# Kernel tuning notes

Hardware: AMD Instinct MI355X
Metric: run time of the kernel (lower is better)

Reference implementation:

```python
import jax, jax.numpy as jnp
import numpy as np

HIDDEN = 1024
NUM_HEADS = 16
HEAD_DIM = HIDDEN // NUM_HEADS
ROPE_BASE = 10000.0
LN_EPS = 1e-8


def _rope_cos_sin(seq_len, dim, dtype=jnp.float32):
    inv_freq = 1.0 / (ROPE_BASE ** (jnp.arange(0, dim, 2, dtype=jnp.float32) / dim))
    t = jnp.arange(seq_len, dtype=jnp.float32)
    freqs = jnp.einsum('i,j->ij', t, inv_freq)          # [S, dim/2]
    emb = jnp.concatenate([freqs, freqs], axis=-1)       # [S, dim]
    return jnp.cos(emb).astype(dtype), jnp.sin(emb).astype(dtype)


def _rotate_half(x):
    x1, x2 = jnp.split(x, 2, axis=-1)
    return jnp.concatenate([-x2, x1], axis=-1)


def setup_inputs() -> dict:
    key = jax.random.key(0)
    ks = jax.random.split(key, 8)
    B, S, H = 4, 2048, HIDDEN
    x = jax.random.normal(ks[0], (B, S, H), dtype=jnp.float32)
    # causal mask, True = attend
    attn_mask = jnp.tril(jnp.ones((S, S), dtype=bool))[None].repeat(B, axis=0)
    lim_p = 1.0 / np.sqrt(H)
    Wp = jax.random.uniform(ks[1], (H, 4 * H), minval=-lim_p, maxval=lim_p, dtype=jnp.float32)
    bp = jax.random.uniform(ks[2], (4 * H,), minval=-lim_p, maxval=lim_p, dtype=jnp.float32)
    ln_g = jnp.ones((H,), dtype=jnp.float32)
    ln_b = jnp.zeros((H,), dtype=jnp.float32)
    Wt = jax.random.uniform(ks[3], (H, H), minval=-lim_p, maxval=lim_p, dtype=jnp.float32)
    bt = jax.random.uniform(ks[4], (H,), minval=-lim_p, maxval=lim_p, dtype=jnp.float32)
    return {"x": x, "attn_mask": attn_mask, "Wp": Wp, "bp": bp,
            "ln_g": ln_g, "ln_b": ln_b, "Wt": Wt, "bt": bt}


def reference(x, attn_mask, Wp, bp, ln_g, ln_b, Wt, bt):
    B, S, H = x.shape
    nh, hd = NUM_HEADS, HEAD_DIM
    proj = x @ Wp + bp                                   # [B,S,4H]
    U, V, Q, K = jnp.split(proj, 4, axis=-1)
    # [B, nh, S, hd]
    Q = Q.reshape(B, S, nh, hd).transpose(0, 2, 1, 3)
    K = K.reshape(B, S, nh, hd).transpose(0, 2, 1, 3)
    V = V.reshape(B, S, nh, hd).transpose(0, 2, 1, 3)
    cos, sin = _rope_cos_sin(S, hd, x.dtype)             # [S, hd]
    Qr = Q * cos + _rotate_half(Q) * sin
    Kr = K * cos + _rotate_half(K) * sin
    scale = hd ** -0.5
    scores = jnp.einsum('bhqd,bhkd->bhqk', Qr, Kr) * scale
    # masked positions -> sigmoid(-inf) == 0; use where for grad safety
    attn = jnp.where(attn_mask[:, None, :, :], jax.nn.sigmoid(scores), 0.0)
    attn_out = jnp.einsum('bhqk,bhkd->bhqd', attn, V)
    attn_out = attn_out.transpose(0, 2, 1, 3).reshape(B, S, H)
    mu = jnp.mean(attn_out, axis=-1, keepdims=True)
    var = jnp.var(attn_out, axis=-1, keepdims=True)
    attn_out = (attn_out - mu) / jnp.sqrt(var + LN_EPS) * ln_g + ln_b
    gated = jax.nn.silu(U) * attn_out
    out = gated @ Wt + bt
    return x + out
```

## Files before the change

### kernel.cpp

```cpp
#include <hip/hip_runtime.h>
#include <math.h>

#define H 1024
#define NH 16
#define HD 64
#define B_ 4
#define S_ 2048
#define ROWS (B_*S_)

#define QSCALE (-0.1803368801111664f)

typedef __bf16 bf16x2_t __attribute__((ext_vector_type(2)));
typedef __bf16 bf16x4_t __attribute__((ext_vector_type(4)));
typedef __bf16 bf16x8_t __attribute__((ext_vector_type(8)));
typedef float floatx4_t __attribute__((ext_vector_type(4)));

#define GLOAD_LDS16(gp, lp)                                                        \
    __builtin_amdgcn_global_load_lds(                                              \
        (const __attribute__((address_space(1))) unsigned int*)(gp),               \
        (__attribute__((address_space(3))) unsigned int*)(lp), 16, 0, 0)

__global__ __launch_bounds__(256)
void convert_x(const float* __restrict__ src, __bf16* __restrict__ dst)
{
    int i = blockIdx.x * blockDim.x + threadIdx.x;
    float4 v = *reinterpret_cast<const float4*>(&src[(size_t)i * 4]);
    bf16x4_t w = { (__bf16)v.x, (__bf16)v.y, (__bf16)v.z, (__bf16)v.w };
    *reinterpret_cast<bf16x4_t*>(&dst[(size_t)i * 4]) = w;
}

__global__ __launch_bounds__(256)
void transpose_cvt(const float* __restrict__ W, __bf16* __restrict__ Wt, int K, int N)
{
    __shared__ __bf16 t[32][33];
    const int tx = threadIdx.x & 31, ty = threadIdx.x >> 5;
    const int bn = blockIdx.x * 32, bk = blockIdx.y * 32;
#pragma unroll
    for (int i = 0; i < 4; i++) {
        int r = ty + i * 8;
        t[tx][r] = (__bf16)W[(size_t)(bk + r) * N + bn + tx];
    }
    __syncthreads();
#pragma unroll
    for (int i = 0; i < 4; i++) {
        int r = ty + i * 8;
        Wt[(size_t)(bn + r) * K + bk + tx] = t[r][tx];
    }
}

template<typename OUT_T, bool RESID>
__global__ __launch_bounds__(256)
void gemm_mfma(const __bf16* __restrict__ A, const __bf16* __restrict__ Bt,
               const float* __restrict__ bias, const float* __restrict__ resid,
               OUT_T* __restrict__ C, int M, int N, int K)
{
    __shared__ __bf16 As[128 * 32];
    __shared__ __bf16 Bs[128 * 32];

    const int tid  = threadIdx.x;
    const int wave = tid >> 6, lane = tid & 63;
    const int quad = lane >> 4, ln = lane & 15;
    const int wm = wave & 1, wn = wave >> 1;
    const int m0 = blockIdx.y * 128, n0 = blockIdx.x * 128;

    const int srow = lane >> 2;
    const int skc  = (lane & 3) * 8;

    floatx4_t acc[4][4];
#pragma unroll
    for (int i = 0; i < 4; i++)
#pragma unroll
        for (int j = 0; j < 4; j++) acc[i][j] = (floatx4_t){0.f, 0.f, 0.f, 0.f};

    for (int k0 = 0; k0 < K; k0 += 32) {
#pragma unroll
        for (int p = 0; p < 2; p++) {
            int i = wave * 2 + p;
            int rl = i * 16 + srow;
            GLOAD_LDS16(A  + (size_t)(m0 + rl) * K + k0 + skc, &As[i * 512]);
            GLOAD_LDS16(Bt + (size_t)(n0 + rl) * K + k0 + skc, &Bs[i * 512]);
        }
        __syncthreads();

        bf16x8_t af[4], bf[4];
#pragma unroll
        for (int mt = 0; mt < 4; mt++)
            af[mt] = *reinterpret_cast<const bf16x8_t*>(&As[(wm * 64 + mt * 16 + ln) * 32 + quad * 8]);
#pragma unroll
        for (int nt = 0; nt < 4; nt++)
            bf[nt] = *reinterpret_cast<const bf16x8_t*>(&Bs[(wn * 64 + nt * 16 + ln) * 32 + quad * 8]);
#pragma unroll
        for (int mt = 0; mt < 4; mt++)
#pragma unroll
            for (int nt = 0; nt < 4; nt++)
                acc[mt][nt] = __builtin_amdgcn_mfma_f32_16x16x32_bf16(af[mt], bf[nt], acc[mt][nt], 0, 0, 0);
        __syncthreads();
    }

#pragma unroll
    for (int mt = 0; mt < 4; mt++) {
#pragma unroll
        for (int nt = 0; nt < 4; nt++) {
            int col = n0 + wn * 64 + nt * 16 + ln;
            float bv = bias[col];
#pragma unroll
            for (int reg = 0; reg < 4; reg++) {
                int row = m0 + wm * 64 + mt * 16 + quad * 4 + reg;
                float v = acc[mt][nt][reg] + bv;
                if (RESID) v += resid[(size_t)row * N + col];
                C[(size_t)row * N + col] = (OUT_T)v;
            }
        }
    }
}

__global__ __launch_bounds__(256)
void reshape_rope(const __bf16* __restrict__ proj,
                  __bf16* __restrict__ Qh, __bf16* __restrict__ Kh,
                  __bf16* __restrict__ VtG)
{
    const int tid = threadIdx.x;
    const int st = blockIdx.x, h = blockIdx.y, b = blockIdx.z;
    const int s0 = st * 64;
    const int bh = b * NH + h;

    {
        const int r = tid >> 2, c = (tid & 3) * 8;
        const int s = s0 + r;
        const size_t inrow  = ((size_t)(b * S_ + s)) * 4096 + h * 64;
        const size_t outrow = ((size_t)(bh * S_ + s)) * 64;
        float cs[8], sn[8];
#pragma unroll
        for (int j = 0; j < 8; j++) {
            int d = c + j;
            float inv = __expf(-(float)d * (9.210340371976184f / 32.0f));
            float ang = (float)s * inv;
            __sincosf(ang, &sn[j], &cs[j]);
        }
        {
            bf16x8_t lo = *reinterpret_cast<const bf16x8_t*>(&proj[inrow + 2048 + c]);
            bf16x8_t hi = *reinterpret_cast<const bf16x8_t*>(&proj[inrow + 2048 + c + 32]);
            bf16x8_t olo, ohi;
#pragma unroll
            for (int j = 0; j < 8; j++) {
                float a = (float)lo[j], bb = (float)hi[j];
                olo[j] = (__bf16)((a * cs[j] - bb * sn[j]) * QSCALE);
                ohi[j] = (__bf16)((bb * cs[j] + a * sn[j]) * QSCALE);
            }
            *reinterpret_cast<bf16x8_t*>(&Qh[outrow + c])      = olo;
            *reinterpret_cast<bf16x8_t*>(&Qh[outrow + c + 32]) = ohi;
        }
        {
            bf16x8_t lo = *reinterpret_cast<const bf16x8_t*>(&proj[inrow + 3072 + c]);
            bf16x8_t hi = *reinterpret_cast<const bf16x8_t*>(&proj[inrow + 3072 + c + 32]);
            bf16x8_t olo, ohi;
#pragma unroll
            for (int j = 0; j < 8; j++) {
                float a = (float)lo[j], bb = (float)hi[j];
                olo[j] = (__bf16)(a * cs[j] - bb * sn[j]);
                ohi[j] = (__bf16)(bb * cs[j] + a * sn[j]);
            }
            *reinterpret_cast<bf16x8_t*>(&Kh[outrow + c])      = olo;
            *reinterpret_cast<bf16x8_t*>(&Kh[outrow + c + 32]) = ohi;
        }
    }

    {
        const int d = tid & 63, k16 = tid >> 6;
        __bf16 vals[16];
#pragma unroll
        for (int j = 0; j < 16; j++) {
            int k = s0 + k16 * 16 + j;
            vals[j] = proj[((size_t)(b * S_ + k)) * 4096 + 1024 + h * 64 + d];
        }
        size_t orow = ((size_t)(bh * 64 + d)) * S_ + s0 + k16 * 16;
        *reinterpret_cast<bf16x8_t*>(&VtG[orow])     = *reinterpret_cast<bf16x8_t*>(&vals[0]);
        *reinterpret_cast<bf16x8_t*>(&VtG[orow + 8]) = *reinterpret_cast<bf16x8_t*>(&vals[8]);
    }
}

__global__ __launch_bounds__(256)
void attn_mfma(const __bf16* __restrict__ Qh, const __bf16* __restrict__ Kh,
               const __bf16* __restrict__ VtG, __bf16* __restrict__ attn_out)
{
    __shared__ __bf16 Ks[4096];
    __shared__ __bf16 Vt[4096];
    __shared__ __bf16 Ps[4][32][72];

    const int tid = threadIdx.x, wave = tid >> 6, lane = tid & 63;
    const int quad = lane >> 4, ln = lane & 15;
    const int qt = (S_ / 128 - 1) - (blockIdx.x >> 6);
    const int hb = blockIdx.x & 63, h = hb & 15, b = hb >> 4, bh = b * NH + h;
    const int Q0 = qt * 128, T0 = 2 * qt;
    const int wl = wave * 16 + ln;

    const size_t qr = ((size_t)bh * S_ + Q0 + wl) * 64;
    bf16x8_t qa[2][2];
    qa[0][0] = *reinterpret_cast<const bf16x8_t*>(&Qh[qr + quad * 8]);
    qa[0][1] = *reinterpret_cast<const bf16x8_t*>(&Qh[qr + 32 + quad * 8]);
    qa[1][0] = *reinterpret_cast<const bf16x8_t*>(&Qh[qr + 4096 + quad * 8]);
    qa[1][1] = *reinterpret_cast<const bf16x8_t*>(&Qh[qr + 4096 + 32 + quad * 8]);

    const int sr = lane >> 3, scl = (lane & 7) ^ sr;
    const int c0 = wave * 2, c1 = c0 + 1;
    const size_t khead = (size_t)bh * S_ * 64;
    const int koff0 = (c0 * 8 + sr) * 64 + scl * 8;
    const int koff1 = (c1 * 8 + sr) * 64 + scl * 8;
    const size_t vg0 = ((size_t)bh * 64 + c0 * 8 + sr) * S_ + scl * 8;
    const size_t vg1 = ((size_t)bh * 64 + c1 * 8 + sr) * S_ + scl * 8;

    const int m7 = ln & 7;
    int ka[4][2];
#pragma unroll
    for (int nt = 0; nt < 4; nt++) {
        int row = nt * 16 + ln;
        ka[nt][0] = row * 64 + ((quad ^ m7) << 3);
        ka[nt][1] = row * 64 + (((quad + 4) ^ m7) << 3);
    }

    floatx4_t o[2][4];
#pragma unroll
    for (int s = 0; s < 2; s++)
#pragma unroll
        for (int dt = 0; dt < 4; dt++) o[s][dt] = (floatx4_t){0.f, 0.f, 0.f, 0.f};

    for (int kt = 0; kt <= T0 + 1; kt++) {
        __syncthreads();
        const size_t kg = khead + (size_t)kt * 4096;
        GLOAD_LDS16(Kh  + kg + koff0, &Ks[c0 * 512]);
        GLOAD_LDS16(Kh  + kg + koff1, &Ks[c1 * 512]);
        GLOAD_LDS16(VtG + vg0 + kt * 64, &Vt[c0 * 512]);
        GLOAD_LDS16(VtG + vg1 + kt * 64, &Vt[c1 * 512]);
        __syncthreads();

        bf16x8_t kf[4][2];
#pragma unroll
        for (int nt = 0; nt < 4; nt++) {
            kf[nt][0] = *reinterpret_cast<const bf16x8_t*>(&Ks[ka[nt][0]]);
            kf[nt][1] = *reinterpret_cast<const bf16x8_t*>(&Ks[ka[nt][1]]);
        }
        bf16x8_t vf[4][2];
#pragma unroll
        for (int dt = 0; dt < 4; dt++) {
            vf[dt][0] = *reinterpret_cast<const bf16x8_t*>(&Vt[ka[dt][0]]);
            vf[dt][1] = *reinterpret_cast<const bf16x8_t*>(&Vt[ka[dt][1]]);
        }

        const int mode0 = (kt < T0) ? 0 : ((kt == T0) ? 1 : 2);
        const int mode1 = (kt <= T0) ? 0 : 1;

#pragma unroll
        for (int s = 0; s < 2; s++) {
            const int mode = s ? mode1 : mode0;
            if (mode == 2) continue;

            floatx4_t st[4];
#pragma unroll
            for (int nt = 0; nt < 4; nt++) {
                floatx4_t acc = (floatx4_t){0.f, 0.f, 0.f, 0.f};
                acc = __builtin_amdgcn_mfma_f32_16x16x32_bf16(kf[nt][0], qa[s][0], acc, 0, 0, 0);
                acc = __builtin_amdgcn_mfma_f32_16x16x32_bf16(kf[nt][1], qa[s][1], acc, 0, 0, 0);
                st[nt] = acc;
            }

#pragma unroll
            for (int nt = 0; nt < 4; nt++) {
                bf16x4_t pk;
#pragma unroll
                for (int r = 0; r < 4; r++) {
                    float a = st[nt][r];
                    if (mode == 1) {
                        int kl = nt * 16 + quad * 4 + r;
                        a = (kl <= wl) ? a : __builtin_inff();
                    }
                    float p = __builtin_amdgcn_rcpf(1.f + __builtin_amdgcn_exp2f(a));
                    pk[r] = (__bf16)p;
                }
                *reinterpret_cast<bf16x4_t*>(&Ps[wave][s * 16 + ln][nt * 16 + quad * 4]) = pk;
            }

            const __bf16* prow = &Ps[wave][s * 16 + ln][quad * 8];
            bf16x8_t p0 = *reinterpret_cast<const bf16x8_t*>(prow);
            bf16x8_t p1 = *reinterpret_cast<const bf16x8_t*>(prow + 32);
#pragma unroll
            for (int dt = 0; dt < 4; dt++) {
                o[s][dt] = __builtin_amdgcn_mfma_f32_16x16x32_bf16(p0, vf[dt][0], o[s][dt], 0, 0, 0);
                o[s][dt] = __builtin_amdgcn_mfma_f32_16x16x32_bf16(p1, vf[dt][1], o[s][dt], 0, 0, 0);
            }
        }
    }

#pragma unroll
    for (int s = 0; s < 2; s++) {
        const int qrow_g = b * S_ + Q0 + s * 64 + wave * 16 + quad * 4;
#pragma unroll
        for (int dt = 0; dt < 4; dt++) {
#pragma unroll
            for (int reg = 0; reg < 4; reg++) {
                attn_out[(size_t)(qrow_g + reg) * H + h * 64 + dt * 16 + ln] =
                    (__bf16)o[s][dt][reg];
            }
        }
    }
}

__global__ __launch_bounds__(256)
void ln_gate_kernel(const __bf16* __restrict__ attn_out, const __bf16* __restrict__ proj,
                    const float* __restrict__ ln_g, const float* __restrict__ ln_b,
                    __bf16* __restrict__ gated)
{
    const int row = blockIdx.x;
    const int tid = threadIdx.x;

    bf16x4_t vb = *reinterpret_cast<const bf16x4_t*>(&attn_out[(size_t)row * H + tid * 4]);
    float v0 = (float)vb[0], v1 = (float)vb[1], v2 = (float)vb[2], v3 = (float)vb[3];
    float s  = v0 + v1 + v2 + v3;
    float sq = v0 * v0 + v1 * v1 + v2 * v2 + v3 * v3;
#pragma unroll
    for (int off = 32; off > 0; off >>= 1) {
        s  += __shfl_down(s, off);
        sq += __shfl_down(sq, off);
    }
    __shared__ float ps[4], pq[4];
    int wave = tid >> 6, lane = tid & 63;
    if (lane == 0) { ps[wave] = s; pq[wave] = sq; }
    __syncthreads();
    float ts = ps[0] + ps[1] + ps[2] + ps[3];
    float tq = pq[0] + pq[1] + pq[2] + pq[3];
    float mu  = ts * (1.f / (float)H);
    float var = tq * (1.f / (float)H) - mu * mu;
    float rstd = rsqrtf(var + 1e-8f);

    bf16x4_t ub = *reinterpret_cast<const bf16x4_t*>(&proj[(size_t)row * 4096 + tid * 4]);
    float4 g  = *reinterpret_cast<const float4*>(&ln_g[tid * 4]);
    float4 bb = *reinterpret_cast<const float4*>(&ln_b[tid * 4]);
    float u0 = (float)ub[0], u1 = (float)ub[1], u2 = (float)ub[2], u3 = (float)ub[3];
    bf16x4_t outv;
    outv[0] = (__bf16)(((v0 - mu) * rstd * g.x + bb.x) * (u0 / (1.f + __expf(-u0))));
    outv[1] = (__bf16)(((v1 - mu) * rstd * g.y + bb.y) * (u1 / (1.f + __expf(-u1))));
    outv[2] = (__bf16)(((v2 - mu) * rstd * g.z + bb.z) * (u2 / (1.f + __expf(-u2))));
    outv[3] = (__bf16)(((v3 - mu) * rstd * g.w + bb.w) * (u3 / (1.f + __expf(-u3))));
    *reinterpret_cast<bf16x4_t*>(&gated[(size_t)row * H + tid * 4]) = outv;
}

extern "C" void kernel_launch(void* const* d_in, const int* in_sizes, int n_in,
                              void* d_out, int out_size, void* d_ws, size_t ws_size,
                              hipStream_t stream)
{
    const float* x    = (const float*)d_in[0];
    const float* Wp   = (const float*)d_in[2];
    const float* bp   = (const float*)d_in[3];
    const float* ln_g = (const float*)d_in[4];
    const float* ln_b = (const float*)d_in[5];
    const float* Wt   = (const float*)d_in[6];
    const float* bt   = (const float*)d_in[7];
    float* out = (float*)d_out;

    char* ws = (char*)d_ws;
    __bf16* proj_bf = (__bf16*)(ws);
    __bf16* attn    = (__bf16*)(ws + (size_t)64  * 1024 * 1024);
    __bf16* gated   = (__bf16*)(ws + (size_t)80  * 1024 * 1024);
    __bf16* VtG     = gated;
    __bf16* Ax      = (__bf16*)(ws + (size_t)96  * 1024 * 1024);
    __bf16* Qh      = Ax;
    __bf16* Kh      = (__bf16*)(ws + (size_t)112 * 1024 * 1024);
    __bf16* Wp_t    = (__bf16*)(ws + (size_t)128 * 1024 * 1024);
    __bf16* Wt_t    = (__bf16*)(ws + (size_t)136 * 1024 * 1024);

    convert_x<<<(ROWS * H / 4) / 256, 256, 0, stream>>>(x, Ax);
    transpose_cvt<<<dim3(4096 / 32, 1024 / 32), 256, 0, stream>>>(Wp, Wp_t, 1024, 4096);
    transpose_cvt<<<dim3(1024 / 32, 1024 / 32), 256, 0, stream>>>(Wt, Wt_t, 1024, 1024);

    dim3 g1(4096 / 128, ROWS / 128);
    gemm_mfma<__bf16, false><<<g1, 256, 0, stream>>>(Ax, Wp_t, bp, nullptr, proj_bf, ROWS, 4096, 1024);

    reshape_rope<<<dim3(S_ / 64, NH, B_), 256, 0, stream>>>(proj_bf, Qh, Kh, VtG);

    attn_mfma<<<(S_ / 128) * NH * B_, 256, 0, stream>>>(Qh, Kh, VtG, attn);

    ln_gate_kernel<<<ROWS, 256, 0, stream>>>(attn, proj_bf, ln_g, ln_b, gated);

    dim3 g3(1024 / 128, ROWS / 128);
    gemm_mfma<float, true><<<g3, 256, 0, stream>>>(gated, Wt_t, bt, x, out, ROWS, 1024, 1024);
}
```

Before: 367.1 us.

## Fuse RoPE and head reshape into projection GEMM epilogue, swizzle LDS

The projection GEMM epilogue now writes U, V, Q and K directly in per-head layouts, applying RoPE and the Q scale in registers. This removes the full re-read of the 64MB proj buffer that the reshape_rope kernel used to do. A small transpose_v kernel remains to build the transposed V. Both GEMMs also XOR-swizzle the LDS k-chunk offsets to reduce bank conflicts. In exchange, the epilogue stores are scalar 2-byte writes spread across strided rows, and each row recomputes sincos.

```diff
diff --git a/kernel.cpp b/kernel.cpp
--- a/kernel.cpp
+++ b/kernel.cpp
@@ -9,6 +9,7 @@
 #define ROWS (B_*S_)
 
 #define QSCALE (-0.1803368801111664f)
+#define ROPE_C (9.210340371976184f / 32.0f)
 
 typedef __bf16 bf16x2_t __attribute__((ext_vector_type(2)));
 typedef __bf16 bf16x4_t __attribute__((ext_vector_type(4)));
@@ -48,11 +49,11 @@
     }
 }
 
-template<typename OUT_T, bool RESID>
-__global__ __launch_bounds__(256)
-void gemm_mfma(const __bf16* __restrict__ A, const __bf16* __restrict__ Bt,
-               const float* __restrict__ bias, const float* __restrict__ resid,
-               OUT_T* __restrict__ C, int M, int N, int K)
+
+__global__ __launch_bounds__(256)
+void gemm_out(const __bf16* __restrict__ A, const __bf16* __restrict__ Bt,
+              const float* __restrict__ bias, const float* __restrict__ resid,
+              float* __restrict__ C, int M, int N, int K)
 {
     __shared__ __bf16 As[128 * 32];
     __shared__ __bf16 Bs[128 * 32];
@@ -64,7 +65,8 @@
     const int m0 = blockIdx.y * 128, n0 = blockIdx.x * 128;
 
     const int srow = lane >> 2;
-    const int skc  = (lane & 3) * 8;
+    const int skc  = (((lane & 3) ^ ((srow >> 1) & 3)) * 8);
+    const int qsw  = (quad ^ ((ln >> 1) & 3)) * 8;
 
     floatx4_t acc[4][4];
 #pragma unroll
@@ -85,10 +87,10 @@
         bf16x8_t af[4], bf[4];
 #pragma unroll
         for (int mt = 0; mt < 4; mt++)
-            af[mt] = *reinterpret_cast<const bf16x8_t*>(&As[(wm * 64 + mt * 16 + ln) * 32 + quad * 8]);
+            af[mt] = *reinterpret_cast<const bf16x8_t*>(&As[(wm * 64 + mt * 16 + ln) * 32 + qsw]);
 #pragma unroll
         for (int nt = 0; nt < 4; nt++)
-            bf[nt] = *reinterpret_cast<const bf16x8_t*>(&Bs[(wn * 64 + nt * 16 + ln) * 32 + quad * 8]);
+            bf[nt] = *reinterpret_cast<const bf16x8_t*>(&Bs[(wn * 64 + nt * 16 + ln) * 32 + qsw]);
 #pragma unroll
         for (int mt = 0; mt < 4; mt++)
 #pragma unroll
@@ -106,77 +108,138 @@
 #pragma unroll
             for (int reg = 0; reg < 4; reg++) {
                 int row = m0 + wm * 64 + mt * 16 + quad * 4 + reg;
-                float v = acc[mt][nt][reg] + bv;
-                if (RESID) v += resid[(size_t)row * N + col];
-                C[(size_t)row * N + col] = (OUT_T)v;
-            }
-        }
-    }
-}
-
-__global__ __launch_bounds__(256)
-void reshape_rope(const __bf16* __restrict__ proj,
-                  __bf16* __restrict__ Qh, __bf16* __restrict__ Kh,
-                  __bf16* __restrict__ VtG)
+                float v = acc[mt][nt][reg] + bv + resid[(size_t)row * N + col];
+                C[(size_t)row * N + col] = v;
+            }
+        }
+    }
+}
+
+__global__ __launch_bounds__(256)
+void gemm_proj(const __bf16* __restrict__ A, const __bf16* __restrict__ Bt,
+               const float* __restrict__ bias,
+               __bf16* __restrict__ Ug, __bf16* __restrict__ Vh,
+               __bf16* __restrict__ Qh, __bf16* __restrict__ Kh)
+{
+    const int M = ROWS, N = 4096, K = 1024;
+    __shared__ __bf16 As[128 * 32];
+    __shared__ __bf16 Bs[128 * 32];
+
+    const int tid  = threadIdx.x;
+    const int wave = tid >> 6, lane = tid & 63;
+    const int quad = lane >> 4, ln = lane & 15;
+    const int wm = wave & 1, wn = wave >> 1;
+    const int m0 = blockIdx.y * 128, n0 = blockIdx.x * 128;
+
+    const int srow = lane >> 2;
+    const int skc  = (((lane & 3) ^ ((srow >> 1) & 3)) * 8);
+    const int qsw  = (quad ^ ((ln >> 1) & 3)) * 8;
+
+    floatx4_t acc[4][4];
+#pragma unroll
+    for (int i = 0; i < 4; i++)
+#pragma unroll
+        for (int j = 0; j < 4; j++) acc[i][j] = (floatx4_t){0.f, 0.f, 0.f, 0.f};
+
+    for (int k0 = 0; k0 < K; k0 += 32) {
+#pragma unroll
+        for (int p = 0; p < 2; p++) {
+            int i = wave * 2 + p;
+            int rl = i * 16 + srow;
+            GLOAD_LDS16(A  + (size_t)(m0 + rl) * K + k0 + skc, &As[i * 512]);
+            GLOAD_LDS16(Bt + (size_t)(n0 + rl) * K + k0 + skc, &Bs[i * 512]);
+        }
+        __syncthreads();
+
+        bf16x8_t af[4], bf[4];
+#pragma unroll
+        for (int mt = 0; mt < 4; mt++)
+            af[mt] = *reinterpret_cast<const bf16x8_t*>(&As[(wm * 64 + mt * 16 + ln) * 32 + qsw]);
+#pragma unroll
+        for (int nt = 0; nt < 4; nt++)
+            bf[nt] = *reinterpret_cast<const bf16x8_t*>(&Bs[(wn * 64 + nt * 16 + ln) * 32 + qsw]);
+#pragma unroll
+        for (int mt = 0; mt < 4; mt++)
+#pragma unroll
+            for (int nt = 0; nt < 4; nt++)
+                acc[mt][nt] = __builtin_amdgcn_mfma_f32_16x16x32_bf16(af[mt], bf[nt], acc[mt][nt], 0, 0, 0);
+        __syncthreads();
+    }
+
+    float bv[4];
+#pragma unroll
+    for (int nt = 0; nt < 4; nt++) bv[nt] = bias[n0 + wn * 64 + nt * 16 + ln];
+
+    if (n0 < 1024) {
+#pragma unroll
+        for (int mt = 0; mt < 4; mt++)
+#pragma unroll
+            for (int nt = 0; nt < 4; nt++) {
+                int col = n0 + wn * 64 + nt * 16 + ln;
+#pragma unroll
+                for (int reg = 0; reg < 4; reg++) {
+                    int row = m0 + wm * 64 + mt * 16 + quad * 4 + reg;
+                    Ug[(size_t)row * 1024 + col] = (__bf16)(acc[mt][nt][reg] + bv[nt]);
+                }
+            }
+    } else if (n0 < 2048) {
+        const int h = ((n0 - 1024) >> 6) + wn;
+#pragma unroll
+        for (int mt = 0; mt < 4; mt++)
+#pragma unroll
+            for (int reg = 0; reg < 4; reg++) {
+                int row = m0 + wm * 64 + mt * 16 + quad * 4 + reg;
+                int b = row >> 11, s = row & (S_ - 1);
+                size_t orow = ((size_t)(b * NH + h) * S_ + s) * 64;
+#pragma unroll
+                for (int nt = 0; nt < 4; nt++)
+                    Vh[orow + nt * 16 + ln] = (__bf16)(acc[mt][nt][reg] + bv[nt]);
+            }
+    } else {
+        const bool isQ = (n0 < 3072);
+        const int h = ((n0 - (isQ ? 2048 : 3072)) >> 6) + wn;
+        __bf16* dst = isQ ? Qh : Kh;
+        const float sc = isQ ? QSCALE : 1.0f;
+        const float inv0 = __expf(-(float)ln * ROPE_C);
+        const float inv1 = __expf(-(float)(16 + ln) * ROPE_C);
+#pragma unroll
+        for (int mt = 0; mt < 4; mt++)
+#pragma unroll
+            for (int reg = 0; reg < 4; reg++) {
+                int row = m0 + wm * 64 + mt * 16 + quad * 4 + reg;
+                int b = row >> 11, s = row & (S_ - 1);
+                size_t orow = ((size_t)(b * NH + h) * S_ + s) * 64;
+                float sn0, cs0, sn1, cs1;
+                __sincosf((float)s * inv0, &sn0, &cs0);
+                __sincosf((float)s * inv1, &sn1, &cs1);
+                float lo0 = acc[0][0][reg], hi0 = acc[0][2][reg];
+                float lo1 = acc[0][1][reg], hi1 = acc[0][3][reg];
+                lo0 = acc[mt][0][reg] + bv[0]; hi0 = acc[mt][2][reg] + bv[2];
+                lo1 = acc[mt][1][reg] + bv[1]; hi1 = acc[mt][3][reg] + bv[3];
+                dst[orow + ln]      = (__bf16)((lo0 * cs0 - hi0 * sn0) * sc);
+                dst[orow + 32 + ln] = (__bf16)((hi0 * cs0 + lo0 * sn0) * sc);
+                dst[orow + 16 + ln] = (__bf16)((lo1 * cs1 - hi1 * sn1) * sc);
+                dst[orow + 48 + ln] = (__bf16)((hi1 * cs1 + lo1 * sn1) * sc);
+            }
+    }
+}
+
+__global__ __launch_bounds__(256)
+void transpose_v(const __bf16* __restrict__ Vh, __bf16* __restrict__ VtG)
 {
     const int tid = threadIdx.x;
-    const int st = blockIdx.x, h = blockIdx.y, b = blockIdx.z;
+    const int st = blockIdx.x, bh = blockIdx.y;
     const int s0 = st * 64;
-    const int bh = b * NH + h;
-
-    {
-        const int r = tid >> 2, c = (tid & 3) * 8;
-        const int s = s0 + r;
-        const size_t inrow  = ((size_t)(b * S_ + s)) * 4096 + h * 64;
-        const size_t outrow = ((size_t)(bh * S_ + s)) * 64;
-        float cs[8], sn[8];
-#pragma unroll
-        for (int j = 0; j < 8; j++) {
-            int d = c + j;
-            float inv = __expf(-(float)d * (9.210340371976184f / 32.0f));
-            float ang = (float)s * inv;
-            __sincosf(ang, &sn[j], &cs[j]);
-        }
-        {
-            bf16x8_t lo = *reinterpret_cast<const bf16x8_t*>(&proj[inrow + 2048 + c]);
-            bf16x8_t hi = *reinterpret_cast<const bf16x8_t*>(&proj[inrow + 2048 + c + 32]);
-            bf16x8_t olo, ohi;
-#pragma unroll
-            for (int j = 0; j < 8; j++) {
-                float a = (float)lo[j], bb = (float)hi[j];
-                olo[j] = (__bf16)((a * cs[j] - bb * sn[j]) * QSCALE);
-                ohi[j] = (__bf16)((bb * cs[j] + a * sn[j]) * QSCALE);
-            }
-            *reinterpret_cast<bf16x8_t*>(&Qh[outrow + c])      = olo;
-            *reinterpret_cast<bf16x8_t*>(&Qh[outrow + c + 32]) = ohi;
-        }
-        {
-            bf16x8_t lo = *reinterpret_cast<const bf16x8_t*>(&proj[inrow + 3072 + c]);
-            bf16x8_t hi = *reinterpret_cast<const bf16x8_t*>(&proj[inrow + 3072 + c + 32]);
-            bf16x8_t olo, ohi;
-#pragma unroll
-            for (int j = 0; j < 8; j++) {
-                float a = (float)lo[j], bb = (float)hi[j];
-                olo[j] = (__bf16)(a * cs[j] - bb * sn[j]);
-                ohi[j] = (__bf16)(bb * cs[j] + a * sn[j]);
-            }
-            *reinterpret_cast<bf16x8_t*>(&Kh[outrow + c])      = olo;
-            *reinterpret_cast<bf16x8_t*>(&Kh[outrow + c + 32]) = ohi;
-        }
-    }
-
-    {
-        const int d = tid & 63, k16 = tid >> 6;
-        __bf16 vals[16];
-#pragma unroll
-        for (int j = 0; j < 16; j++) {
-            int k = s0 + k16 * 16 + j;
-            vals[j] = proj[((size_t)(b * S_ + k)) * 4096 + 1024 + h * 64 + d];
-        }
-        size_t orow = ((size_t)(bh * 64 + d)) * S_ + s0 + k16 * 16;
-        *reinterpret_cast<bf16x8_t*>(&VtG[orow])     = *reinterpret_cast<bf16x8_t*>(&vals[0]);
-        *reinterpret_cast<bf16x8_t*>(&VtG[orow + 8]) = *reinterpret_cast<bf16x8_t*>(&vals[8]);
-    }
+    const int d = tid & 63, k16 = tid >> 6;
+    __bf16 vals[16];
+#pragma unroll
+    for (int j = 0; j < 16; j++) {
+        int k = s0 + k16 * 16 + j;
+        vals[j] = Vh[((size_t)bh * S_ + k) * 64 + d];
+    }
+    size_t orow = ((size_t)(bh * 64 + d)) * S_ + s0 + k16 * 16;
+    *reinterpret_cast<bf16x8_t*>(&VtG[orow])     = *reinterpret_cast<bf16x8_t*>(&vals[0]);
+    *reinterpret_cast<bf16x8_t*>(&VtG[orow + 8]) = *reinterpret_cast<bf16x8_t*>(&vals[8]);
 }
 
 __global__ __launch_bounds__(256)
@@ -305,7 +368,7 @@
 }
 
 __global__ __launch_bounds__(256)
-void ln_gate_kernel(const __bf16* __restrict__ attn_out, const __bf16* __restrict__ proj,
+void ln_gate_kernel(const __bf16* __restrict__ attn_out, const __bf16* __restrict__ Ug,
                     const float* __restrict__ ln_g, const float* __restrict__ ln_b,
                     __bf16* __restrict__ gated)
 {
@@ -331,7 +394,7 @@
     float var = tq * (1.f / (float)H) - mu * mu;
     float rstd = rsqrtf(var + 1e-8f);
 
-    bf16x4_t ub = *reinterpret_cast<const bf16x4_t*>(&proj[(size_t)row * 4096 + tid * 4]);
+    bf16x4_t ub = *reinterpret_cast<const bf16x4_t*>(&Ug[(size_t)row * 1024 + tid * 4]);
     float4 g  = *reinterpret_cast<const float4*>(&ln_g[tid * 4]);
     float4 bb = *reinterpret_cast<const float4*>(&ln_b[tid * 4]);
     float u0 = (float)ub[0], u1 = (float)ub[1], u2 = (float)ub[2], u3 = (float)ub[3];
@@ -357,29 +420,31 @@
     float* out = (float*)d_out;
 
     char* ws = (char*)d_ws;
-    __bf16* proj_bf = (__bf16*)(ws);
-    __bf16* attn    = (__bf16*)(ws + (size_t)64  * 1024 * 1024);
-    __bf16* gated   = (__bf16*)(ws + (size_t)80  * 1024 * 1024);
-    __bf16* VtG     = gated;
-    __bf16* Ax      = (__bf16*)(ws + (size_t)96  * 1024 * 1024);
-    __bf16* Qh      = Ax;
-    __bf16* Kh      = (__bf16*)(ws + (size_t)112 * 1024 * 1024);
-    __bf16* Wp_t    = (__bf16*)(ws + (size_t)128 * 1024 * 1024);
-    __bf16* Wt_t    = (__bf16*)(ws + (size_t)136 * 1024 * 1024);
+    const size_t MB = 1024 * 1024;
+    __bf16* Ug    = (__bf16*)(ws);
+    __bf16* Vh    = (__bf16*)(ws + 16  * MB);
+    __bf16* Qh    = (__bf16*)(ws + 32  * MB);
+    __bf16* Kh    = (__bf16*)(ws + 48  * MB);
+    __bf16* attn  = (__bf16*)(ws + 64  * MB);
+    __bf16* gated = (__bf16*)(ws + 80  * MB);
+    __bf16* VtG   = (__bf16*)(ws + 96  * MB);
+    __bf16* Ax    = (__bf16*)(ws + 112 * MB);
+    __bf16* Wp_t  = (__bf16*)(ws + 128 * MB);
+    __bf16* Wt_t  = (__bf16*)(ws + 136 * MB);
 
     convert_x<<<(ROWS * H / 4) / 256, 256, 0, stream>>>(x, Ax);
     transpose_cvt<<<dim3(4096 / 32, 1024 / 32), 256, 0, stream>>>(Wp, Wp_t, 1024, 4096);
     transpose_cvt<<<dim3(1024 / 32, 1024 / 32), 256, 0, stream>>>(Wt, Wt_t, 1024, 1024);
 
     dim3 g1(4096 / 128, ROWS / 128);
-    gemm_mfma<__bf16, false><<<g1, 256, 0, stream>>>(Ax, Wp_t, bp, nullptr, proj_bf, ROWS, 4096, 1024);
-
-    reshape_rope<<<dim3(S_ / 64, NH, B_), 256, 0, stream>>>(proj_bf, Qh, Kh, VtG);
+    gemm_proj<<<g1, 256, 0, stream>>>(Ax, Wp_t, bp, Ug, Vh, Qh, Kh);
+
+    transpose_v<<<dim3(S_ / 64, B_ * NH), 256, 0, stream>>>(Vh, VtG);
 
     attn_mfma<<<(S_ / 128) * NH * B_, 256, 0, stream>>>(Qh, Kh, VtG, attn);
 
-    ln_gate_kernel<<<ROWS, 256, 0, stream>>>(attn, proj_bf, ln_g, ln_b, gated);
+    ln_gate_kernel<<<ROWS, 256, 0, stream>>>(attn, Ug, ln_g, ln_b, gated);
 
     dim3 g3(1024 / 128, ROWS / 128);
-    gemm_mfma<float, true><<<g3, 256, 0, stream>>>(gated, Wt_t, bt, x, out, ROWS, 1024, 1024);
-}
+    gemm_out<<<g3, 256, 0, stream>>>(gated, Wt_t, bt, x, out, ROWS, 1024, 1024);
+}
```

Result: faster. 345.2 us (-6.0%).
